# Kernel optimization log

Hardware: AMD Instinct MI355X
Metric: run time of the kernel (lower is better)

## Reference

```python
import jax, jax.numpy as jnp
import numpy as np

N_NODES = 10000
N_EDGES = 640000
NFEAT = 128
NHID = 128
NCLASS = 40
DROP = 0.5


def setup_inputs() -> dict:
    key = jax.random.key(0)
    ks = jax.random.split(key, 12)
    inp = {
        "x": jax.random.normal(ks[0], (N_NODES, NFEAT), dtype=jnp.float32),
        "edge_index": jax.random.randint(ks[1], (2, N_EDGES), 0, N_NODES, dtype=jnp.int64),
        "W0": jax.random.normal(ks[2], (NHID, NFEAT), dtype=jnp.float32) * (1.0 / np.sqrt(NFEAT)),
        "b0": jax.random.normal(ks[3], (NHID,), dtype=jnp.float32) * 0.01,
        "W1": jax.random.normal(ks[4], (NHID, NHID), dtype=jnp.float32) * (1.0 / np.sqrt(NHID)),
        "b1": jax.random.normal(ks[5], (NHID,), dtype=jnp.float32) * 0.01,
        "W2": jax.random.normal(ks[6], (NHID, NHID), dtype=jnp.float32) * (1.0 / np.sqrt(NHID)),
        "b2": jax.random.normal(ks[7], (NHID,), dtype=jnp.float32) * 0.01,
        "p_drop": jnp.full((NHID,), DROP, dtype=jnp.float32),
        "Wl": jax.random.normal(ks[8], (NCLASS, NHID), dtype=jnp.float32) * (1.0 / np.sqrt(NHID)),
        "bl": jax.random.normal(ks[9], (NCLASS,), dtype=jnp.float32) * 0.01,
    }
    return inp


def reference(x, edge_index, W0, b0, W1, b1, W2, b2, p_drop, Wl, bl):
    src = edge_index[0]
    dst = edge_index[1]
    # deterministic variational dropout mask (shared across layers)
    mask = jnp.clip(p_drop, 0.0, 1.0)[None, :]  # [1, nhid]
    h = x
    for W, b in ((W0, b0), (W1, b1), (W2, b2)):
        # GINConv, eps=0: h_i' = Linear(h_i + sum_{j->i} h_j)
        agg = jax.ops.segment_sum(h[src], dst, num_segments=N_NODES)  # [N, d]
        h = (h + agg) @ W.T + b
        h = jax.nn.relu(h) * mask
    return h @ Wl.T + bl
```

## Files before the change

### kernel.cpp

```cpp
#include <hip/hip_runtime.h>

#define NN 10000
#define NE 640000
#define D 128
#define NC 40
#define CAP 128
#define NBKT 313
#define BCAP 2304

typedef unsigned short u16;
typedef unsigned int u32;
typedef short bf16x8 __attribute__((ext_vector_type(8)));
typedef float f32x4v __attribute__((ext_vector_type(4)));

__device__ __forceinline__ float bf2f(u16 u) { return __uint_as_float(((u32)u) << 16); }
__device__ __forceinline__ u16 f2bf(float f) {
    u32 u = __float_as_uint(f);
    u += 0x7fff + ((u >> 16) & 1);
    return (u16)(u >> 16);
}
__device__ __forceinline__ void upadd(u32 w, float& a, float& b) {
    a += __uint_as_float(w << 16);
    b += __uint_as_float(w & 0xffff0000u);
}

__global__ __launch_bounds__(256) void zero_kernel(uint4* __restrict__ p, int n4) {
    int i = blockIdx.x * 256 + threadIdx.x;
    if (i < n4) p[i] = make_uint4(0u, 0u, 0u, 0u);
}

__global__ __launch_bounds__(256) void phaseA(const float* __restrict__ x,
        const int* __restrict__ src, const int* __restrict__ dst,
        const float* __restrict__ W0, const float* __restrict__ W1, const float* __restrict__ W2,
        int* __restrict__ gcur, u32* __restrict__ gbucket,
        u16* __restrict__ whi, u16* __restrict__ wlo, u16* __restrict__ G) {
    __shared__ union {
        struct { u32 bin[NBKT][16]; int bcnt[NBKT]; int gbase[NBKT]; u32 ovf[128][2]; int ocnt; } a;
        u16 Gs[32 * 128];
    } sm;
    int b = blockIdx.x, t = threadIdx.x;
    if (b < 625) {
        for (int i = t; i < NBKT; i += 256) sm.a.bcnt[i] = 0;
        if (t == 0) sm.a.ocnt = 0;
        __syncthreads();
        int e0 = b * 1024 + t * 4;
        int4 d4 = *reinterpret_cast<const int4*>(dst + e0);
        int4 s4 = *reinterpret_cast<const int4*>(src + e0);
        int dd[4] = {d4.x, d4.y, d4.z, d4.w};
        int ss[4] = {s4.x, s4.y, s4.z, s4.w};
        #pragma unroll
        for (int i = 0; i < 4; i++) {
            int bk = dd[i] >> 5;
            u32 entry = ((u32)(dd[i] & 31) << 16) | (u32)ss[i];
            int pos = atomicAdd(&sm.a.bcnt[bk], 1);
            if (pos < 16) sm.a.bin[bk][pos] = entry;
            else {
                int o = atomicAdd(&sm.a.ocnt, 1);
                if (o < 128) { sm.a.ovf[o][0] = ((u32)bk << 16) | (u32)pos; sm.a.ovf[o][1] = entry; }
            }
        }
        __syncthreads();
        for (int i = t; i < NBKT; i += 256) {
            int n = sm.a.bcnt[i];
            sm.a.gbase[i] = n ? atomicAdd(&gcur[i * 16], n) : 0;
        }
        __syncthreads();
        for (int i = t; i < NBKT; i += 256) {
            int n = sm.a.bcnt[i];
            int m = n > 16 ? 16 : n;
            int base = sm.a.gbase[i];
            for (int j = 0; j < m; j++) {
                int p = base + j;
                if (p < BCAP) gbucket[(size_t)i * BCAP + p] = sm.a.bin[i][j];
            }
        }
        int oc = sm.a.ocnt; if (oc > 128) oc = 128;
        for (int i = t; i < oc; i += 256) {
            int bk = (int)(sm.a.ovf[i][0] >> 16);
            int pos = (int)(sm.a.ovf[i][0] & 0xffff);
            int p = sm.a.gbase[bk] + pos;
            if (p >= 0 && p < BCAP) gbucket[(size_t)bk * BCAP + p] = sm.a.ovf[i][1];
        }
    } else if (b < 938) {
        int nb0 = (b - 625) * 32;
        int wid = t >> 6, l = t & 63;
        int m = l & 15, gq = l >> 4;
        int mt = wid & 1, nh = wid >> 1;
        int nodeA = nb0 + mt * 16 + m;
        if (nodeA >= NN) nodeA = NN - 1;
        const float* xr = x + (size_t)nodeA * 128;
        f32x4v acc[4];
        #pragma unroll
        for (int nt = 0; nt < 4; nt++) acc[nt] = (f32x4v){0.f, 0.f, 0.f, 0.f};
        #pragma unroll
        for (int ks = 0; ks < 4; ks++) {
            float4 a0 = *reinterpret_cast<const float4*>(xr + ks * 32 + gq * 8);
            float4 a1 = *reinterpret_cast<const float4*>(xr + ks * 32 + gq * 8 + 4);
            float av[8] = {a0.x, a0.y, a0.z, a0.w, a1.x, a1.y, a1.z, a1.w};
            union { uint4 u; bf16x8 v; } ca;
            u32 ap[4];
            #pragma unroll
            for (int j = 0; j < 4; j++)
                ap[j] = (u32)f2bf(av[2 * j]) | ((u32)f2bf(av[2 * j + 1]) << 16);
            ca.u = make_uint4(ap[0], ap[1], ap[2], ap[3]);
            #pragma unroll
            for (int nt = 0; nt < 4; nt++) {
                int n = nh * 64 + nt * 16 + m;
                const float* wr = W0 + (size_t)n * 128 + ks * 32 + gq * 8;
                float4 w0 = *reinterpret_cast<const float4*>(wr);
                float4 w1 = *reinterpret_cast<const float4*>(wr + 4);
                float wv[8] = {w0.x, w0.y, w0.z, w0.w, w1.x, w1.y, w1.z, w1.w};
                u32 hp[4], lp[4];
                #pragma unroll
                for (int j = 0; j < 4; j++) {
                    u16 h0 = f2bf(wv[2 * j]), h1 = f2bf(wv[2 * j + 1]);
                    float r0 = wv[2 * j] - bf2f(h0), r1 = wv[2 * j + 1] - bf2f(h1);
                    hp[j] = (u32)h0 | ((u32)h1 << 16);
                    lp[j] = (u32)f2bf(r0) | ((u32)f2bf(r1) << 16);
                }
                union { uint4 u; bf16x8 v; } ch, cl;
                ch.u = make_uint4(hp[0], hp[1], hp[2], hp[3]);
                cl.u = make_uint4(lp[0], lp[1], lp[2], lp[3]);
                acc[nt] = __builtin_amdgcn_mfma_f32_16x16x32_bf16(ca.v, ch.v, acc[nt], 0, 0, 0);
                acc[nt] = __builtin_amdgcn_mfma_f32_16x16x32_bf16(ca.v, cl.v, acc[nt], 0, 0, 0);
            }
        }
        #pragma unroll
        for (int nt = 0; nt < 4; nt++) {
            #pragma unroll
            for (int j = 0; j < 4; j++) {
                int mm = mt * 16 + gq * 4 + j;
                int n = nh * 64 + nt * 16 + m;
                sm.Gs[mm * 128 + (n ^ ((mm & 7) << 4))] = f2bf(acc[nt][j]);
            }
        }
        __syncthreads();
        #pragma unroll
        for (int i = 0; i < 2; i++) {
            int c = t + i * 256;
            int mm = c >> 4, n0 = (c & 15) * 8;
            int node = nb0 + mm;
            if (node < NN) {
                uint4 v = *reinterpret_cast<const uint4*>(&sm.Gs[mm * 128 + (n0 ^ ((mm & 7) << 4))]);
                *reinterpret_cast<uint4*>(G + (size_t)node * 128 + n0) = v;
            }
        }
    } else {
        int idx = (b - 938) * 2048 + t * 8;
        int wi = idx >> 14, off = idx & 16383;
        const float* W = wi ? W2 : W1;
        float4 v0 = *reinterpret_cast<const float4*>(W + off);
        float4 v1 = *reinterpret_cast<const float4*>(W + off + 4);
        float wv[8] = {v0.x, v0.y, v0.z, v0.w, v1.x, v1.y, v1.z, v1.w};
        u16 ho[8], lo[8];
        #pragma unroll
        for (int j = 0; j < 8; j++) {
            u16 h = f2bf(wv[j]);
            ho[j] = h;
            lo[j] = f2bf(wv[j] - bf2f(h));
        }
        *reinterpret_cast<uint4*>(whi + idx + 16384) = *reinterpret_cast<uint4*>(ho);
        *reinterpret_cast<uint4*>(wlo + idx + 16384) = *reinterpret_cast<uint4*>(lo);
    }
}

__global__ __launch_bounds__(256) void phaseB(const int* __restrict__ gcur,
        const u32* __restrict__ gbucket, u16* __restrict__ csr, int* __restrict__ cnt) {
    __shared__ u16 slice[32 * CAP];
    __shared__ int scnt[32];
    int b = blockIdx.x, t = threadIdx.x;
    if (t < 32) scnt[t] = 0;
    __syncthreads();
    int total = gcur[b * 16];
    if (total > BCAP) total = BCAP;
    for (int i = t; i < total; i += 256) {
        u32 e = gbucket[(size_t)b * BCAP + i];
        int dl = (int)((e >> 16) & 31);
        int pos = atomicAdd(&scnt[dl], 1);
        if (pos < CAP) slice[dl * CAP + pos] = (u16)(e & 0xffff);
    }
    __syncthreads();
    int node0 = b * 32;
    const u32* s32 = reinterpret_cast<const u32*>(slice);
    u32* c32 = reinterpret_cast<u32*>(csr) + (size_t)node0 * 64;
    for (int i = t; i < 2048; i += 256) {
        if (node0 + (i >> 6) < NN) c32[i] = s32[i];
    }
    if (t < 32) {
        int node = node0 + t;
        if (node < NN) cnt[node] = scnt[t] > CAP ? CAP : scnt[t];
    }
}

template<bool LAST>
__global__ __launch_bounds__(1024) void fuse_kernel(
        const u16* __restrict__ gin, const int* __restrict__ cnt, const u16* __restrict__ csr,
        const float* __restrict__ bias, const float* __restrict__ pd,
        const u16* __restrict__ wh, const u16* __restrict__ wl_, u16* __restrict__ gout,
        const float* __restrict__ Wl, const float* __restrict__ bl, float* __restrict__ out) {
    __shared__ u16 nbr[16][128];
    __shared__ union {
        u16 A[16 * 128];
        struct { float WlS[NC * 129]; float rows[16 * D]; float blS[NC]; } c;
    } sm;
    const int t = threadIdx.x, wid = t >> 6, ln = t & 63;
    const int q = ln >> 4, fq = ln & 15, fo8 = fq << 3;
    const int nb0 = blockIdx.x * 16;
    const int node = nb0 + wid;

    if (LAST) {
        for (int i = t; i < NC * D; i += 1024) sm.c.WlS[(i >> 7) * 129 + (i & 127)] = Wl[i];
        if (t < NC) sm.c.blS[t] = bl[t];
    }

    int c_ = cnt[node];
    if (c_ > CAP) c_ = CAP;
    *reinterpret_cast<u32*>(&nbr[wid][ln << 1]) =
        *reinterpret_cast<const u32*>(csr + ((size_t)node << 7) + (ln << 1));

    float va[8] = {0.f, 0.f, 0.f, 0.f, 0.f, 0.f, 0.f, 0.f};
    if (q == 0) {
        uint4 v = *reinterpret_cast<const uint4*>(gin + ((size_t)node << 7) + fo8);
        upadd(v.x, va[0], va[1]); upadd(v.y, va[2], va[3]);
        upadd(v.z, va[4], va[5]); upadd(v.w, va[6], va[7]);
    }
    int iters = (c_ + 15) >> 4;
    for (int i = 0; i < iters; i++) {
        int base = (i << 4) + (q << 2);
        ushort4 ids = *reinterpret_cast<const ushort4*>(&nbr[wid][base]);
        int id0 = (base + 0 < c_) ? (int)ids.x : node;
        int id1 = (base + 1 < c_) ? (int)ids.y : node;
        int id2 = (base + 2 < c_) ? (int)ids.z : node;
        int id3 = (base + 3 < c_) ? (int)ids.w : node;
        uint4 v0 = *reinterpret_cast<const uint4*>(gin + ((size_t)id0 << 7) + fo8);
        uint4 v1 = *reinterpret_cast<const uint4*>(gin + ((size_t)id1 << 7) + fo8);
        uint4 v2 = *reinterpret_cast<const uint4*>(gin + ((size_t)id2 << 7) + fo8);
        uint4 v3 = *reinterpret_cast<const uint4*>(gin + ((size_t)id3 << 7) + fo8);
        if (base + 0 < c_) {
            upadd(v0.x, va[0], va[1]); upadd(v0.y, va[2], va[3]);
            upadd(v0.z, va[4], va[5]); upadd(v0.w, va[6], va[7]);
        }
        if (base + 1 < c_) {
            upadd(v1.x, va[0], va[1]); upadd(v1.y, va[2], va[3]);
            upadd(v1.z, va[4], va[5]); upadd(v1.w, va[6], va[7]);
        }
        if (base + 2 < c_) {
            upadd(v2.x, va[0], va[1]); upadd(v2.y, va[2], va[3]);
            upadd(v2.z, va[4], va[5]); upadd(v2.w, va[6], va[7]);
        }
        if (base + 3 < c_) {
            upadd(v3.x, va[0], va[1]); upadd(v3.y, va[2], va[3]);
            upadd(v3.z, va[4], va[5]); upadd(v3.w, va[6], va[7]);
        }
    }
    #pragma unroll
    for (int j = 0; j < 8; j++) {
        va[j] += __shfl_xor(va[j], 16);
        va[j] += __shfl_xor(va[j], 32);
    }
    if (ln < 16) {
        float4 bv0 = *reinterpret_cast<const float4*>(bias + fo8);
        float4 bv1 = *reinterpret_cast<const float4*>(bias + fo8 + 4);
        float4 mv0 = *reinterpret_cast<const float4*>(pd + fo8);
        float4 mv1 = *reinterpret_cast<const float4*>(pd + fo8 + 4);
        float bb[8] = {bv0.x, bv0.y, bv0.z, bv0.w, bv1.x, bv1.y, bv1.z, bv1.w};
        float mm[8] = {mv0.x, mv0.y, mv0.z, mv0.w, mv1.x, mv1.y, mv1.z, mv1.w};
        float r[8];
        #pragma unroll
        for (int j = 0; j < 8; j++) {
            float mk = fminf(fmaxf(mm[j], 0.f), 1.f);
            r[j] = fmaxf(va[j] + bb[j], 0.f) * mk;
        }
        if (LAST) {
            #pragma unroll
            for (int j = 0; j < 8; j++) sm.c.rows[wid * D + fo8 + j] = r[j];
        } else {
            u32 p0 = (u32)f2bf(r[0]) | ((u32)f2bf(r[1]) << 16);
            u32 p1 = (u32)f2bf(r[2]) | ((u32)f2bf(r[3]) << 16);
            u32 p2 = (u32)f2bf(r[4]) | ((u32)f2bf(r[5]) << 16);
            u32 p3 = (u32)f2bf(r[6]) | ((u32)f2bf(r[7]) << 16);
            *reinterpret_cast<uint4*>(&sm.A[wid * 128 + ((fq ^ (wid & 7)) << 3)]) =
                make_uint4(p0, p1, p2, p3);
        }
    }
    __syncthreads();

    if (LAST) {
        if (t < 16 * NC) {
            int n = t / NC, c = t - n * NC;
            const float* rr = &sm.c.rows[n * D];
            const float* wr = &sm.c.WlS[c * 129];
            float acc = sm.c.blS[c];
            #pragma unroll 8
            for (int k = 0; k < D; k++) acc = fmaf(rr[k], wr[k], acc);
            out[(size_t)(nb0 + n) * NC + c] = acc;
        }
        return;
    }

    int m = ln & 15, gq = ln >> 4;
    bf16x8 afr[4];
    if (wid < 8) {
        #pragma unroll
        for (int ks = 0; ks < 4; ks++) {
            int chunk = gq + ks * 4;
            afr[ks] = *reinterpret_cast<const bf16x8*>(&sm.A[m * 128 + ((chunk ^ (m & 7)) << 3)]);
        }
    }
    __syncthreads();
    if (wid < 8) {
        f32x4v acc = (f32x4v){0.f, 0.f, 0.f, 0.f};
        int n = wid * 16 + m;
        const u16* whp = wh + (size_t)n * 128;
        const u16* wlp = wl_ + (size_t)n * 128;
        #pragma unroll
        for (int ks = 0; ks < 4; ks++) {
            bf16x8 bh = *reinterpret_cast<const bf16x8*>(whp + ks * 32 + gq * 8);
            bf16x8 bl = *reinterpret_cast<const bf16x8*>(wlp + ks * 32 + gq * 8);
            acc = __builtin_amdgcn_mfma_f32_16x16x32_bf16(afr[ks], bh, acc, 0, 0, 0);
            acc = __builtin_amdgcn_mfma_f32_16x16x32_bf16(afr[ks], bl, acc, 0, 0, 0);
        }
        u16* Gs = sm.A;
        #pragma unroll
        for (int j = 0; j < 4; j++) {
            int mm = gq * 4 + j;
            Gs[mm * 128 + (n ^ ((mm & 7) << 4))] = f2bf(acc[j]);
        }
    }
    __syncthreads();
    if (t < 256) {
        const u16* Gs = sm.A;
        int mm = t >> 4, n0 = (t & 15) * 8;
        uint4 v = *reinterpret_cast<const uint4*>(&Gs[mm * 128 + (n0 ^ ((mm & 7) << 4))]);
        *reinterpret_cast<uint4*>(gout + (size_t)(nb0 + mm) * 128 + n0) = v;
    }
}

extern "C" void kernel_launch(void* const* d_in, const int* in_sizes, int n_in,
                              void* d_out, int out_size, void* d_ws, size_t ws_size,
                              hipStream_t stream) {
    const float* x  = (const float*)d_in[0];
    const int*   ei = (const int*)d_in[1];
    const float* W0 = (const float*)d_in[2];
    const float* b0 = (const float*)d_in[3];
    const float* W1 = (const float*)d_in[4];
    const float* b1 = (const float*)d_in[5];
    const float* W2 = (const float*)d_in[6];
    const float* b2 = (const float*)d_in[7];
    const float* pd = (const float*)d_in[8];
    const float* Wl = (const float*)d_in[9];
    const float* bl = (const float*)d_in[10];

    char* ws = (char*)d_ws;
    int* gcur    = (int*)ws;
    int* cnt     = (int*)(ws + 20480);
    u16* csr     = (u16*)(ws + 61440);
    u16* gbA     = (u16*)(ws + 2621440);
    u16* gbB     = (u16*)(ws + 5181440);
    u32* gbucket = (u32*)(ws + 5181440);
    u16* whi     = (u16*)(ws + 8066048);
    u16* wlo     = (u16*)(ws + 8164352);

    const int* src = ei;
    const int* dst = ei + NE;

    zero_kernel<<<5, 256, 0, stream>>>((uint4*)gcur, 1280);
    phaseA<<<954, 256, 0, stream>>>(x, src, dst, W0, W1, W2, gcur, gbucket, whi, wlo, gbA);
    phaseB<<<NBKT, 256, 0, stream>>>(gcur, gbucket, csr, cnt);
    fuse_kernel<false><<<625, 1024, 0, stream>>>(gbA, cnt, csr, b0, pd,
                                                 whi + 16384, wlo + 16384, gbB,
                                                 nullptr, nullptr, nullptr);
    fuse_kernel<false><<<625, 1024, 0, stream>>>(gbB, cnt, csr, b1, pd,
                                                 whi + 32768, wlo + 32768, gbA,
                                                 nullptr, nullptr, nullptr);
    fuse_kernel<true><<<625, 1024, 0, stream>>>(gbA, cnt, csr, b2, pd,
                                                nullptr, nullptr, nullptr,
                                                Wl, bl, (float*)d_out);
}
```

Measured before the change: 114.3 us.

## Coarsen edge binning blocks and double neighbor gathers per iteration

The edge-binning stage now uses 157 blocks that each handle 4096 edges instead of 625 blocks of 1024. Shared bins grow to depth 24, so each block issues fewer global atomics per bucket and writes longer contiguous runs. The bucket flush is restructured so each thread writes one flat slot rather than looping over a whole bucket. Separately, the aggregation loop in the fused kernel issues 8 neighbor row loads per iteration instead of 4, exposing more memory-level parallelism at the cost of more registers. The larger bins raise shared memory per block, and an overflow beyond 128 entries per block would silently drop edges.

```diff
diff --git a/kernel.cpp b/kernel.cpp
--- a/kernel.cpp
+++ b/kernel.cpp
@@ -7,6 +7,8 @@
 #define CAP 128
 #define NBKT 313
 #define BCAP 2304
+#define NBIN 157
+#define DEPTH 24
 
 typedef unsigned short u16;
 typedef unsigned int u32;
@@ -35,28 +37,33 @@
         int* __restrict__ gcur, u32* __restrict__ gbucket,
         u16* __restrict__ whi, u16* __restrict__ wlo, u16* __restrict__ G) {
     __shared__ union {
-        struct { u32 bin[NBKT][16]; int bcnt[NBKT]; int gbase[NBKT]; u32 ovf[128][2]; int ocnt; } a;
+        struct { u32 bin[NBKT][DEPTH]; int bcnt[NBKT]; int gbase[NBKT]; u32 ovf[128][2]; int ocnt; } a;
         u16 Gs[32 * 128];
     } sm;
     int b = blockIdx.x, t = threadIdx.x;
-    if (b < 625) {
+    if (b < NBIN) {
         for (int i = t; i < NBKT; i += 256) sm.a.bcnt[i] = 0;
         if (t == 0) sm.a.ocnt = 0;
         __syncthreads();
-        int e0 = b * 1024 + t * 4;
-        int4 d4 = *reinterpret_cast<const int4*>(dst + e0);
-        int4 s4 = *reinterpret_cast<const int4*>(src + e0);
-        int dd[4] = {d4.x, d4.y, d4.z, d4.w};
-        int ss[4] = {s4.x, s4.y, s4.z, s4.w};
-        #pragma unroll
-        for (int i = 0; i < 4; i++) {
-            int bk = dd[i] >> 5;
-            u32 entry = ((u32)(dd[i] & 31) << 16) | (u32)ss[i];
-            int pos = atomicAdd(&sm.a.bcnt[bk], 1);
-            if (pos < 16) sm.a.bin[bk][pos] = entry;
-            else {
-                int o = atomicAdd(&sm.a.ocnt, 1);
-                if (o < 128) { sm.a.ovf[o][0] = ((u32)bk << 16) | (u32)pos; sm.a.ovf[o][1] = entry; }
+        #pragma unroll
+        for (int rep = 0; rep < 4; rep++) {
+            int e0 = b * 4096 + rep * 1024 + t * 4;
+            if (e0 < NE) {
+                int4 d4 = *reinterpret_cast<const int4*>(dst + e0);
+                int4 s4 = *reinterpret_cast<const int4*>(src + e0);
+                int dd[4] = {d4.x, d4.y, d4.z, d4.w};
+                int ss[4] = {s4.x, s4.y, s4.z, s4.w};
+                #pragma unroll
+                for (int i = 0; i < 4; i++) {
+                    int bk = dd[i] >> 5;
+                    u32 entry = ((u32)(dd[i] & 31) << 16) | (u32)ss[i];
+                    int pos = atomicAdd(&sm.a.bcnt[bk], 1);
+                    if (pos < DEPTH) sm.a.bin[bk][pos] = entry;
+                    else {
+                        int o = atomicAdd(&sm.a.ocnt, 1);
+                        if (o < 128) { sm.a.ovf[o][0] = ((u32)bk << 16) | (u32)pos; sm.a.ovf[o][1] = entry; }
+                    }
+                }
             }
         }
         __syncthreads();
@@ -65,13 +72,12 @@
             sm.a.gbase[i] = n ? atomicAdd(&gcur[i * 16], n) : 0;
         }
         __syncthreads();
-        for (int i = t; i < NBKT; i += 256) {
-            int n = sm.a.bcnt[i];
-            int m = n > 16 ? 16 : n;
-            int base = sm.a.gbase[i];
-            for (int j = 0; j < m; j++) {
-                int p = base + j;
-                if (p < BCAP) gbucket[(size_t)i * BCAP + p] = sm.a.bin[i][j];
+        for (int idx = t; idx < NBKT * DEPTH; idx += 256) {
+            int bk = idx / DEPTH, j = idx - bk * DEPTH;
+            int n = sm.a.bcnt[bk];
+            if (j < (n > DEPTH ? DEPTH : n)) {
+                int p = sm.a.gbase[bk] + j;
+                if (p < BCAP) gbucket[(size_t)bk * BCAP + p] = sm.a.bin[bk][j];
             }
         }
         int oc = sm.a.ocnt; if (oc > 128) oc = 128;
@@ -81,8 +87,8 @@
             int p = sm.a.gbase[bk] + pos;
             if (p >= 0 && p < BCAP) gbucket[(size_t)bk * BCAP + p] = sm.a.ovf[i][1];
         }
-    } else if (b < 938) {
-        int nb0 = (b - 625) * 32;
+    } else if (b < NBIN + 313) {
+        int nb0 = (b - NBIN) * 32;
         int wid = t >> 6, l = t & 63;
         int m = l & 15, gq = l >> 4;
         int mt = wid & 1, nh = wid >> 1;
@@ -146,7 +152,7 @@
             }
         }
     } else {
-        int idx = (b - 938) * 2048 + t * 8;
+        int idx = (b - (NBIN + 313)) * 2048 + t * 8;
         int wi = idx >> 14, off = idx & 16383;
         const float* W = wi ? W2 : W1;
         float4 v0 = *reinterpret_cast<const float4*>(W + off);
@@ -224,34 +230,36 @@
         upadd(v.x, va[0], va[1]); upadd(v.y, va[2], va[3]);
         upadd(v.z, va[4], va[5]); upadd(v.w, va[6], va[7]);
     }
-    int iters = (c_ + 15) >> 4;
+    int iters = (c_ + 31) >> 5;
     for (int i = 0; i < iters; i++) {
-        int base = (i << 4) + (q << 2);
-        ushort4 ids = *reinterpret_cast<const ushort4*>(&nbr[wid][base]);
-        int id0 = (base + 0 < c_) ? (int)ids.x : node;
-        int id1 = (base + 1 < c_) ? (int)ids.y : node;
-        int id2 = (base + 2 < c_) ? (int)ids.z : node;
-        int id3 = (base + 3 < c_) ? (int)ids.w : node;
+        int b0 = (i << 5) + (q << 2);
+        int b1 = b0 + 16;
+        ushort4 ia = *reinterpret_cast<const ushort4*>(&nbr[wid][b0]);
+        ushort4 ib = *reinterpret_cast<const ushort4*>(&nbr[wid][b1]);
+        int id0 = (b0 + 0 < c_) ? (int)ia.x : node;
+        int id1 = (b0 + 1 < c_) ? (int)ia.y : node;
+        int id2 = (b0 + 2 < c_) ? (int)ia.z : node;
+        int id3 = (b0 + 3 < c_) ? (int)ia.w : node;
+        int id4 = (b1 + 0 < c_) ? (int)ib.x : node;
+        int id5 = (b1 + 1 < c_) ? (int)ib.y : node;
+        int id6 = (b1 + 2 < c_) ? (int)ib.z : node;
+        int id7 = (b1 + 3 < c_) ? (int)ib.w : node;
         uint4 v0 = *reinterpret_cast<const uint4*>(gin + ((size_t)id0 << 7) + fo8);
         uint4 v1 = *reinterpret_cast<const uint4*>(gin + ((size_t)id1 << 7) + fo8);
         uint4 v2 = *reinterpret_cast<const uint4*>(gin + ((size_t)id2 << 7) + fo8);
         uint4 v3 = *reinterpret_cast<const uint4*>(gin + ((size_t)id3 << 7) + fo8);
-        if (base + 0 < c_) {
-            upadd(v0.x, va[0], va[1]); upadd(v0.y, va[2], va[3]);
-            upadd(v0.z, va[4], va[5]); upadd(v0.w, va[6], va[7]);
-        }
-        if (base + 1 < c_) {
-            upadd(v1.x, va[0], va[1]); upadd(v1.y, va[2], va[3]);
-            upadd(v1.z, va[4], va[5]); upadd(v1.w, va[6], va[7]);
-        }
-        if (base + 2 < c_) {
-            upadd(v2.x, va[0], va[1]); upadd(v2.y, va[2], va[3]);
-            upadd(v2.z, va[4], va[5]); upadd(v2.w, va[6], va[7]);
-        }
-        if (base + 3 < c_) {
-            upadd(v3.x, va[0], va[1]); upadd(v3.y, va[2], va[3]);
-            upadd(v3.z, va[4], va[5]); upadd(v3.w, va[6], va[7]);
-        }
+        uint4 v4 = *reinterpret_cast<const uint4*>(gin + ((size_t)id4 << 7) + fo8);
+        uint4 v5 = *reinterpret_cast<const uint4*>(gin + ((size_t)id5 << 7) + fo8);
+        uint4 v6 = *reinterpret_cast<const uint4*>(gin + ((size_t)id6 << 7) + fo8);
+        uint4 v7 = *reinterpret_cast<const uint4*>(gin + ((size_t)id7 << 7) + fo8);
+        if (b0 + 0 < c_) { upadd(v0.x, va[0], va[1]); upadd(v0.y, va[2], va[3]); upadd(v0.z, va[4], va[5]); upadd(v0.w, va[6], va[7]); }
+        if (b0 + 1 < c_) { upadd(v1.x, va[0], va[1]); upadd(v1.y, va[2], va[3]); upadd(v1.z, va[4], va[5]); upadd(v1.w, va[6], va[7]); }
+        if (b0 + 2 < c_) { upadd(v2.x, va[0], va[1]); upadd(v2.y, va[2], va[3]); upadd(v2.z, va[4], va[5]); upadd(v2.w, va[6], va[7]); }
+        if (b0 + 3 < c_) { upadd(v3.x, va[0], va[1]); upadd(v3.y, va[2], va[3]); upadd(v3.z, va[4], va[5]); upadd(v3.w, va[6], va[7]); }
+        if (b1 + 0 < c_) { upadd(v4.x, va[0], va[1]); upadd(v4.y, va[2], va[3]); upadd(v4.z, va[4], va[5]); upadd(v4.w, va[6], va[7]); }
+        if (b1 + 1 < c_) { upadd(v5.x, va[0], va[1]); upadd(v5.y, va[2], va[3]); upadd(v5.z, va[4], va[5]); upadd(v5.w, va[6], va[7]); }
+        if (b1 + 2 < c_) { upadd(v6.x, va[0], va[1]); upadd(v6.y, va[2], va[3]); upadd(v6.z, va[4], va[5]); upadd(v6.w, va[6], va[7]); }
+        if (b1 + 3 < c_) { upadd(v7.x, va[0], va[1]); upadd(v7.y, va[2], va[3]); upadd(v7.z, va[4], va[5]); upadd(v7.w, va[6], va[7]); }
     }
     #pragma unroll
     for (int j = 0; j < 8; j++) {
@@ -365,7 +373,7 @@
     const int* dst = ei + NE;
 
     zero_kernel<<<5, 256, 0, stream>>>((uint4*)gcur, 1280);
-    phaseA<<<954, 256, 0, stream>>>(x, src, dst, W0, W1, W2, gcur, gbucket, whi, wlo, gbA);
+    phaseA<<<NBIN + 313 + 16, 256, 0, stream>>>(x, src, dst, W0, W1, W2, gcur, gbucket, whi, wlo, gbA);
     phaseB<<<NBKT, 256, 0, stream>>>(gcur, gbucket, csr, cnt);
     fuse_kernel<false><<<625, 1024, 0, stream>>>(gbA, cnt, csr, b0, pd,
                                                  whi + 16384, wlo + 16384, gbB,
```

After: 99.13 us. -13.3%, faster.
